# Optimization experiments

Hardware: AMD Instinct MI355X
Metric: run time of the kernel (lower is better)

The kernel has to match this reference:

```python
import jax, jax.numpy as jnp
import numpy as np


def setup_inputs() -> dict:
    key = jax.random.key(0)
    k1, k2 = jax.random.split(key)
    B, D, H, W = 64, 64, 32, 32
    K = 1024
    z_e = jax.random.normal(k1, (B, D, H, W), dtype=jnp.float32)
    embedding = jax.random.normal(k2, (K, D), dtype=jnp.float32)
    return {"z_e": z_e, "embedding": embedding}


def reference(z_e, embedding):
    # Eval-mode forward of VectorQuantizer (EMA buffer updates are training-only state).
    B, D, H, W = z_e.shape
    K = embedding.shape[0]
    # (N, D) flattened encoder outputs, N = B*H*W
    flat = jnp.transpose(z_e, (0, 2, 3, 1)).reshape(-1, D)
    dist = (jnp.sum(flat * flat, axis=1, keepdims=True)
            + jnp.sum(embedding * embedding, axis=1)
            - 2.0 * flat @ embedding.T)  # (N, K)
    indices = jnp.argmin(dist, axis=1)  # (N,)
    z_q_flat = embedding[indices]  # (N, D) gather
    z_q = jnp.transpose(z_q_flat.reshape(B, H, W, D), (0, 3, 1, 2))
    # commitment loss: mse(z_e, sg(z_q))
    commitment_loss = jnp.mean((z_e - jax.lax.stop_gradient(z_q)) ** 2)
    # straight-through estimator
    z_q = z_e + jax.lax.stop_gradient(z_q - z_e)
    indices_bhw = indices.reshape(B, H, W)
    # fraction of codebook entries used this batch (jit-friendly unique count)
    used = jnp.zeros((K,), dtype=jnp.float32).at[indices].set(1.0)
    codebook_usage = jnp.sum(used) / K
    return z_q, commitment_loss, indices_bhw, codebook_usage
```

## Files before the change

kernel.cpp:

```cpp
#include <hip/hip_runtime.h>


#define DIMS 64
#define K_CODES 1024
#define N_QUERIES 65536
#define HW 1024
#define TOTAL_ELEMS 4194304
#define PLANE 4096

typedef __attribute__((ext_vector_type(8))) short v8s;
typedef __attribute__((ext_vector_type(4))) float f32x4;

__device__ inline unsigned short f2bf(float x) {
    union { float f; unsigned u; } v; v.f = x;
    unsigned r = v.u + 0x7fff + ((v.u >> 16) & 1);
    return (unsigned short)(r >> 16);
}
__device__ inline float bf2f(unsigned short h) {
    union { unsigned u; float f; } v; v.u = ((unsigned)h) << 16; return v.f;
}

__global__ void vq_prep(const float* __restrict__ emb, float* __restrict__ ws_norm,
                        int* __restrict__ ws_flags, float* __restrict__ ws_loss) {
    int k = blockIdx.x * 256 + threadIdx.x;
    const float4* row = (const float4*)(emb + k * DIMS);
    float s = 0.f;
#pragma unroll
    for (int i = 0; i < 16; ++i) {
        float4 v = row[i];
        s += v.x * v.x + v.y * v.y + v.z * v.z + v.w * v.w;
    }
    ws_norm[k] = s;
    ws_flags[k] = 0;
    if (k == 0) *ws_loss = 0.f;
}

#define MFMA16(A_, B_, C_) __builtin_amdgcn_mfma_f32_16x16x32_bf16(A_, B_, C_, 0, 0, 0)

__global__ __launch_bounds__(256, 2)
void vq_main(const float* __restrict__ z_e, const float* __restrict__ emb,
             const float* __restrict__ ws_norm, int* __restrict__ ws_flags,
             float* __restrict__ ws_loss, float* __restrict__ out) {
    __shared__ unsigned short ldsB[2][3 * PLANE];
    __shared__ int   fIdx[128];
    __shared__ float wsum[4];

    const int tid  = threadIdx.x;
    const int lane = tid & 63;
    const int wid  = tid >> 6;
    const int qbase = blockIdx.x * 128;
    const int b    = qbase >> 10;
    const int hwb  = qbase & (HW - 1);

    const int col  = lane & 15;
    const int qd   = lane >> 4;

    v8s afr[2][2][3];
    {
        const float* zb = z_e + b * (DIMS * HW);
#pragma unroll
        for (int rt = 0; rt < 2; ++rt) {
            int hwq = hwb + wid * 32 + rt * 16 + col;
#pragma unroll
            for (int kc = 0; kc < 2; ++kc) {
                int dbase = kc * 32 + qd * 8;
#pragma unroll
                for (int j = 0; j < 8; ++j) {
                    float x = zb[(dbase + j) * HW + hwq];
                    unsigned short h = f2bf(x);  float r1 = x - bf2f(h);
                    unsigned short m = f2bf(r1); float r2 = r1 - bf2f(m);
                    afr[rt][kc][0][j] = (short)h;
                    afr[rt][kc][1][j] = (short)m;
                    afr[rt][kc][2][j] = (short)f2bf(r2);
                }
            }
        }
    }

    float bestv[2][4];
    int   besti[2][4];
#pragma unroll
    for (int rt = 0; rt < 2; ++rt)
#pragma unroll
        for (int r = 0; r < 4; ++r) { bestv[rt][r] = 3.4e38f; besti[rt][r] = 0; }

    float4 regs[4];

    auto stage_loads = [&](int t) {
        const float4* src = (const float4*)(emb + t * 64 * DIMS);
#pragma unroll
        for (int i = 0; i < 4; ++i) regs[i] = src[tid + 256 * i];
    };
    auto stage_write = [&](int bb) {
        unsigned short* dst = &ldsB[bb][0];
#pragma unroll
        for (int i = 0; i < 4; ++i) {
            int e    = (tid + 256 * i) * 4;
            int code = e >> 6;
            int d    = e & 63;
            int o    = d >> 3;
            int sub  = d & 7;
            float xs[4] = {regs[i].x, regs[i].y, regs[i].z, regs[i].w};
            unsigned short h[4], mm_[4], l[4];
#pragma unroll
            for (int q = 0; q < 4; ++q) {
                float x = xs[q];
                unsigned short hh = f2bf(x);  float r1 = x - bf2f(hh);
                unsigned short mh = f2bf(r1); float r2 = r1 - bf2f(mh);
                h[q] = hh; mm_[q] = mh; l[q] = f2bf(r2);
            }
            int base = (o * 64 + code) * 8 + sub;
            uint2 uh, um, ul;
            uh.x = (unsigned)h[0]   | ((unsigned)h[1] << 16);
            uh.y = (unsigned)h[2]   | ((unsigned)h[3] << 16);
            um.x = (unsigned)mm_[0] | ((unsigned)mm_[1] << 16);
            um.y = (unsigned)mm_[2] | ((unsigned)mm_[3] << 16);
            ul.x = (unsigned)l[0]   | ((unsigned)l[1] << 16);
            ul.y = (unsigned)l[2]   | ((unsigned)l[3] << 16);
            *(uint2*)(dst + base)             = uh;
            *(uint2*)(dst + PLANE + base)     = um;
            *(uint2*)(dst + 2 * PLANE + base) = ul;
        }
    };

    stage_loads(0);
    stage_write(0);
    __syncthreads();

    for (int t = 0; t < 16; ++t) {
        const int cur = t & 1;
        if (t < 15) stage_loads(t + 1);
        const unsigned short* bufc = &ldsB[cur][0];
#pragma unroll
        for (int cs = 0; cs < 4; ++cs) {
            float nrm = ws_norm[t * 64 + cs * 16 + col];
            v8s bfr[2][3];
#pragma unroll
            for (int kc = 0; kc < 2; ++kc)
#pragma unroll
                for (int p = 0; p < 3; ++p)
                    bfr[kc][p] = *(const v8s*)(bufc + p * PLANE +
                                 (((kc * 4 + qd) * 64) + cs * 16 + col) * 8);
            f32x4 acc0 = {0.f, 0.f, 0.f, 0.f};
            f32x4 acc1 = {0.f, 0.f, 0.f, 0.f};
#pragma unroll
            for (int kc = 0; kc < 2; ++kc) {
                acc0 = MFMA16(afr[0][kc][0], bfr[kc][0], acc0);
                acc1 = MFMA16(afr[1][kc][0], bfr[kc][0], acc1);
                acc0 = MFMA16(afr[0][kc][0], bfr[kc][1], acc0);
                acc1 = MFMA16(afr[1][kc][0], bfr[kc][1], acc1);
                acc0 = MFMA16(afr[0][kc][1], bfr[kc][0], acc0);
                acc1 = MFMA16(afr[1][kc][1], bfr[kc][0], acc1);
                acc0 = MFMA16(afr[0][kc][1], bfr[kc][1], acc0);
                acc1 = MFMA16(afr[1][kc][1], bfr[kc][1], acc1);
                acc0 = MFMA16(afr[0][kc][0], bfr[kc][2], acc0);
                acc1 = MFMA16(afr[1][kc][0], bfr[kc][2], acc1);
                acc0 = MFMA16(afr[0][kc][2], bfr[kc][0], acc0);
                acc1 = MFMA16(afr[1][kc][2], bfr[kc][0], acc1);
            }
            int cbase = t * 64 + cs * 16 + col;
#pragma unroll
            for (int r = 0; r < 4; ++r) {
                float d0 = fmaf(-2.f, acc0[r], nrm);
                if (d0 < bestv[0][r]) { bestv[0][r] = d0; besti[0][r] = cbase; }
                float d1 = fmaf(-2.f, acc1[r], nrm);
                if (d1 < bestv[1][r]) { bestv[1][r] = d1; besti[1][r] = cbase; }
            }
        }
        if (t < 15) stage_write(1 - cur);
        __syncthreads();
    }

#pragma unroll
    for (int rt = 0; rt < 2; ++rt)
#pragma unroll
    for (int r = 0; r < 4; ++r) {
        float v = bestv[rt][r];
        int   idx = besti[rt][r];
#pragma unroll
        for (int m = 8; m >= 1; m >>= 1) {
            float ov = __shfl_xor(v, m, 64);
            int   oi = __shfl_xor(idx, m, 64);
            if (ov < v || (ov == v && oi < idx)) { v = ov; idx = oi; }
        }
        if (col == 0) {
            int q = wid * 32 + rt * 16 + qd * 4 + r;
            fIdx[q] = idx;
            out[TOTAL_ELEMS + 1 + qbase + q] = (float)idx;
            ws_flags[idx] = 1;
        }
    }
    __syncthreads();

    const int q  = tid & 127;
    const int dh = tid >> 7;
    const int n  = qbase + q;
    const int bb = n >> 10;
    const int hw = n & (HW - 1);
    const int myIdx = fIdx[q];
    const float* erow = emb + myIdx * DIMS;
    float lsum = 0.f;
#pragma unroll
    for (int it = 0; it < 32; ++it) {
        int d = it * 2 + dh;
        float v = erow[d];
        int   o = bb * (DIMS * HW) + d * HW + hw;
        float ze = z_e[o];
        out[o] = v;
        float df = ze - v;
        lsum = fmaf(df, df, lsum);
    }
#pragma unroll
    for (int off = 32; off > 0; off >>= 1) lsum += __shfl_down(lsum, off, 64);
    if (lane == 0) wsum[wid] = lsum;
    __syncthreads();
    if (tid == 0) atomicAdd(ws_loss, wsum[0] + wsum[1] + wsum[2] + wsum[3]);
}

__global__ void vq_final(const int* __restrict__ flags, const float* __restrict__ loss,
                         float* __restrict__ out) {
    __shared__ int cnt[256];
    int tid = threadIdx.x;
    int c = flags[tid] + flags[tid + 256] + flags[tid + 512] + flags[tid + 768];
    cnt[tid] = c;
    __syncthreads();
    for (int s = 128; s > 0; s >>= 1) {
        if (tid < s) cnt[tid] += cnt[tid + s];
        __syncthreads();
    }
    if (tid == 0) {
        out[TOTAL_ELEMS] = *loss / (float)TOTAL_ELEMS;
        out[TOTAL_ELEMS + 1 + N_QUERIES] = (float)cnt[0] / (float)K_CODES;
    }
}

extern "C" void kernel_launch(void* const* d_in, const int* in_sizes, int n_in,
                              void* d_out, int out_size, void* d_ws, size_t ws_size,
                              hipStream_t stream) {
    const float* z_e = (const float*)d_in[0];
    const float* emb = (const float*)d_in[1];
    float* out = (float*)d_out;
    float* ws_norm  = (float*)d_ws;
    int*   ws_flags = (int*)((char*)d_ws + 4096);
    float* ws_loss  = (float*)((char*)d_ws + 8192);

    vq_prep<<<4, 256, 0, stream>>>(emb, ws_norm, ws_flags, ws_loss);
    vq_main<<<512, 256, 0, stream>>>(z_e, emb, ws_norm, ws_flags, ws_loss, out);
    vq_final<<<1, 256, 0, stream>>>(ws_flags, ws_loss, out);
}
```

Baseline: 135.4 us.

## Pre-split codebook once, DMA tiles to LDS, fuse final reduction

```diff
diff --git a/kernel.cpp b/kernel.cpp
--- a/kernel.cpp
+++ b/kernel.cpp
@@ -7,6 +7,11 @@
 #define HW 1024
 #define TOTAL_ELEMS 4194304
 #define PLANE 4096
+#define TILE_SHORTS 12288
+#define TILE_BYTES 24576
+#define SPLIT_OFF 16384
+#define SPLIT_BYTES 393216
+#define NBLK 512
 
 typedef __attribute__((ext_vector_type(8))) short v8s;
 typedef __attribute__((ext_vector_type(4))) float f32x4;
@@ -20,30 +25,63 @@
     union { unsigned u; float f; } v; v.u = ((unsigned)h) << 16; return v.f;
 }
 
+__device__ inline void gload_lds16(const void* g, void* l) {
+    __builtin_amdgcn_global_load_lds(
+        (const __attribute__((address_space(1))) void*)g,
+        (__attribute__((address_space(3))) void*)l, 16, 0, 0);
+}
+
 __global__ void vq_prep(const float* __restrict__ emb, float* __restrict__ ws_norm,
-                        int* __restrict__ ws_flags, float* __restrict__ ws_loss) {
+                        unsigned* __restrict__ ws_flags, float* __restrict__ ws_loss,
+                        int* __restrict__ ws_cnt, unsigned short* __restrict__ ws_split) {
     int k = blockIdx.x * 256 + threadIdx.x;
     const float4* row = (const float4*)(emb + k * DIMS);
+    unsigned short* base = ws_split ? (ws_split + (k >> 6) * TILE_SHORTS + (k & 63) * 8)
+                                    : (unsigned short*)0;
     float s = 0.f;
 #pragma unroll
-    for (int i = 0; i < 16; ++i) {
-        float4 v = row[i];
-        s += v.x * v.x + v.y * v.y + v.z * v.z + v.w * v.w;
+    for (int o = 0; o < 8; ++o) {
+        float4 v0 = row[o * 2], v1 = row[o * 2 + 1];
+        float xs[8] = {v0.x, v0.y, v0.z, v0.w, v1.x, v1.y, v1.z, v1.w};
+        unsigned h[8], m[8], l[8];
+#pragma unroll
+        for (int j = 0; j < 8; ++j) {
+            float x = xs[j];
+            s += x * x;
+            unsigned short hh = f2bf(x);  float r1 = x - bf2f(hh);
+            unsigned short mh = f2bf(r1); float r2 = r1 - bf2f(mh);
+            h[j] = hh; m[j] = mh; l[j] = f2bf(r2);
+        }
+        if (base) {
+            uint4 uh = {h[0] | (h[1] << 16), h[2] | (h[3] << 16),
+                        h[4] | (h[5] << 16), h[6] | (h[7] << 16)};
+            uint4 um = {m[0] | (m[1] << 16), m[2] | (m[3] << 16),
+                        m[4] | (m[5] << 16), m[6] | (m[7] << 16)};
+            uint4 ul = {l[0] | (l[1] << 16), l[2] | (l[3] << 16),
+                        l[4] | (l[5] << 16), l[6] | (l[7] << 16)};
+            *(uint4*)(base + 0 * PLANE + o * 512) = uh;
+            *(uint4*)(base + 1 * PLANE + o * 512) = um;
+            *(uint4*)(base + 2 * PLANE + o * 512) = ul;
+        }
     }
     ws_norm[k] = s;
-    ws_flags[k] = 0;
-    if (k == 0) *ws_loss = 0.f;
+    if (k < 32) ws_flags[k] = 0u;
+    if (k == 0) { *ws_loss = 0.f; *ws_cnt = 0; }
 }
 
 #define MFMA16(A_, B_, C_) __builtin_amdgcn_mfma_f32_16x16x32_bf16(A_, B_, C_, 0, 0, 0)
 
-__global__ __launch_bounds__(256, 2)
+template <bool DMA>
+__global__ __launch_bounds__(256, 3)
 void vq_main(const float* __restrict__ z_e, const float* __restrict__ emb,
-             const float* __restrict__ ws_norm, int* __restrict__ ws_flags,
-             float* __restrict__ ws_loss, float* __restrict__ out) {
+             const float* __restrict__ ws_norm, unsigned* __restrict__ ws_flags,
+             float* __restrict__ ws_loss, int* __restrict__ ws_cnt,
+             const unsigned short* __restrict__ ws_split, float* __restrict__ out) {
     __shared__ unsigned short ldsB[2][3 * PLANE];
-    __shared__ int   fIdx[128];
-    __shared__ float wsum[4];
+    __shared__ int      fIdx[128];
+    __shared__ float    wsum[4];
+    __shared__ unsigned umask[32];
+    __shared__ int      lastBlk;
 
     const int tid  = threadIdx.x;
     const int lane = tid & 63;
@@ -54,6 +92,8 @@
 
     const int col  = lane & 15;
     const int qd   = lane >> 4;
+
+    if (tid < 32) umask[tid] = 0u;
 
     v8s afr[2][2][3];
     {
@@ -84,8 +124,15 @@
 #pragma unroll
         for (int r = 0; r < 4; ++r) { bestv[rt][r] = 3.4e38f; besti[rt][r] = 0; }
 
+    auto stageD = [&](int t, int bb) {
+        const char* g = (const char*)ws_split + t * TILE_BYTES + wid * 6144 + lane * 16;
+        char* l = (char*)(&ldsB[bb][0]) + wid * 6144;
+#pragma unroll
+        for (int j = 0; j < 6; ++j)
+            gload_lds16(g + j * 1024, l + j * 1024);
+    };
+
     float4 regs[4];
-
     auto stage_loads = [&](int t) {
         const float4* src = (const float4*)(emb + t * 64 * DIMS);
 #pragma unroll
@@ -123,13 +170,16 @@
         }
     };
 
-    stage_loads(0);
-    stage_write(0);
+    if constexpr (DMA) { stageD(0, 0); }
+    else               { stage_loads(0); stage_write(0); }
     __syncthreads();
 
     for (int t = 0; t < 16; ++t) {
         const int cur = t & 1;
-        if (t < 15) stage_loads(t + 1);
+        if (t < 15) {
+            if constexpr (DMA) stageD(t + 1, 1 - cur);
+            else               stage_loads(t + 1);
+        }
         const unsigned short* bufc = &ldsB[cur][0];
 #pragma unroll
         for (int cs = 0; cs < 4; ++cs) {
@@ -167,7 +217,7 @@
                 if (d1 < bestv[1][r]) { bestv[1][r] = d1; besti[1][r] = cbase; }
             }
         }
-        if (t < 15) stage_write(1 - cur);
+        if constexpr (!DMA) { if (t < 15) stage_write(1 - cur); }
         __syncthreads();
     }
 
@@ -187,7 +237,7 @@
             int q = wid * 32 + rt * 16 + qd * 4 + r;
             fIdx[q] = idx;
             out[TOTAL_ELEMS + 1 + qbase + q] = (float)idx;
-            ws_flags[idx] = 1;
+            atomicOr(&umask[idx >> 5], 1u << (idx & 31));
         }
     }
     __syncthreads();
@@ -214,23 +264,24 @@
     for (int off = 32; off > 0; off >>= 1) lsum += __shfl_down(lsum, off, 64);
     if (lane == 0) wsum[wid] = lsum;
     __syncthreads();
+
+    if (tid < 32) atomicOr(&ws_flags[tid], umask[tid]);
     if (tid == 0) atomicAdd(ws_loss, wsum[0] + wsum[1] + wsum[2] + wsum[3]);
-}
-
-__global__ void vq_final(const int* __restrict__ flags, const float* __restrict__ loss,
-                         float* __restrict__ out) {
-    __shared__ int cnt[256];
-    int tid = threadIdx.x;
-    int c = flags[tid] + flags[tid + 256] + flags[tid + 512] + flags[tid + 768];
-    cnt[tid] = c;
+    __threadfence();
+    if (tid == 0) lastBlk = (atomicAdd(ws_cnt, 1) == NBLK - 1) ? 1 : 0;
     __syncthreads();
-    for (int s = 128; s > 0; s >>= 1) {
-        if (tid < s) cnt[tid] += cnt[tid + s];
-        __syncthreads();
-    }
-    if (tid == 0) {
-        out[TOTAL_ELEMS] = *loss / (float)TOTAL_ELEMS;
-        out[TOTAL_ELEMS + 1 + N_QUERIES] = (float)cnt[0] / (float)K_CODES;
+    if (lastBlk) {
+        int c = 0;
+        if (tid < 32) c = __popc(atomicOr(&ws_flags[tid], 0u));
+        if (tid < 64) {
+#pragma unroll
+            for (int off = 32; off >= 1; off >>= 1) c += __shfl_down(c, off, 64);
+        }
+        if (tid == 0) {
+            float L = atomicAdd(ws_loss, 0.f);
+            out[TOTAL_ELEMS] = L / (float)TOTAL_ELEMS;
+            out[TOTAL_ELEMS + 1 + N_QUERIES] = (float)c / (float)K_CODES;
+        }
     }
 }
 
@@ -240,11 +291,20 @@
     const float* z_e = (const float*)d_in[0];
     const float* emb = (const float*)d_in[1];
     float* out = (float*)d_out;
-    float* ws_norm  = (float*)d_ws;
-    int*   ws_flags = (int*)((char*)d_ws + 4096);
-    float* ws_loss  = (float*)((char*)d_ws + 8192);
-
-    vq_prep<<<4, 256, 0, stream>>>(emb, ws_norm, ws_flags, ws_loss);
-    vq_main<<<512, 256, 0, stream>>>(z_e, emb, ws_norm, ws_flags, ws_loss, out);
-    vq_final<<<1, 256, 0, stream>>>(ws_flags, ws_loss, out);
-}
+    float*    ws_norm  = (float*)d_ws;
+    unsigned* ws_flags = (unsigned*)((char*)d_ws + 4096);
+    float*    ws_loss  = (float*)((char*)d_ws + 8192);
+    int*      ws_cnt   = (int*)((char*)d_ws + 8256);
+
+    bool dma = ws_size >= (size_t)(SPLIT_OFF + SPLIT_BYTES);
+    unsigned short* ws_split = dma ? (unsigned short*)((char*)d_ws + SPLIT_OFF)
+                                   : (unsigned short*)0;
+
+    vq_prep<<<4, 256, 0, stream>>>(emb, ws_norm, ws_flags, ws_loss, ws_cnt, ws_split);
+    if (dma)
+        vq_main<true><<<NBLK, 256, 0, stream>>>(z_e, emb, ws_norm, ws_flags, ws_loss,
+                                                ws_cnt, ws_split, out);
+    else
+        vq_main<false><<<NBLK, 256, 0, stream>>>(z_e, emb, ws_norm, ws_flags, ws_loss,
+                                                 ws_cnt, ws_split, out);
+}
```

Measured after the change: 176.4 us. +30.3%, slower.
